# Kernel optimization log

Measured on AMD Instinct MI355X. Metric: run time of the kernel, lower is better.

Reference implementation:

```python
import jax, jax.numpy as jnp
import numpy as np

B, S, D, H, NK = 2, 512, 256, 8, 16
DK = D // H
NEG = -1e32


def _layer_norm(x, g, b, eps=1e-5):
    m = jnp.mean(x, axis=-1, keepdims=True)
    v = jnp.var(x, axis=-1, keepdims=True)
    return (x - m) / jnp.sqrt(v + eps) * g + b


def _attention(q, k, v, mask, gamma, maxout):
    # q,k,v: [b,h,s,dk]; mask: [1,1,s,s] bool; gamma: [h,1,1]
    d_k = q.shape[-1]
    scores = jnp.einsum('bhqd,bhkd->bhqk', q, k) / float(np.sqrt(d_k))
    s = scores.shape[-1]
    # gamma exp-decay branch (at=None in practice -> position_effect path)
    sm = jax.nn.softmax(jnp.where(mask, scores, NEG), axis=-1)
    distcum = jnp.cumsum(sm, axis=-1)
    disttotal = jnp.sum(sm, axis=-1, keepdims=True)
    idx = jnp.arange(s, dtype=scores.dtype)
    pos = jnp.abs(idx[None, :] - idx[:, None])[None, None]  # |x1 - x2|
    dist = jax.lax.stop_gradient(
        jnp.sqrt(jnp.clip((disttotal - distcum) * pos, 0.0, None)))
    g = -jnp.abs(gamma)[None]  # [1,h,1,1]
    total_effect = jnp.clip(jnp.exp(dist * g), 1e-5, 1e5)
    scores = scores * total_effect
    scores = jax.nn.softmax(jnp.where(mask, scores, NEG), axis=-1)
    scores = jnp.where(mask, scores, 0.0)
    if maxout:
        scale = jnp.minimum(1.0 / jnp.max(scores, axis=-1, keepdims=True), 5.0)
        scores = scores * scale
    out = jnp.einsum('bhqk,bhkd->bhqd', scores, v)
    return out, scores


def _mha(qx, kx, vx, mask, Wq, bq, Wk, bk, Wv, bv, Wo, bo, gammas, maxout):
    b, s, d = qx.shape
    def proj(x, W, bb):
        return (x @ W.T + bb).reshape(b, s, H, DK).transpose(0, 2, 1, 3)
    q = proj(qx, Wq, bq)
    k = proj(kx, Wk, bk)
    v = proj(vx, Wv, bv)
    out, scores = _attention(q, k, v, mask, gammas, maxout)
    concat = out.transpose(0, 2, 1, 3).reshape(b, s, d)
    return concat @ Wo.T + bo, scores


def _layer(qx, kx, vx, mask, Wq, bq, Wk, bk, Wv, bv, Wo, bo, gammas, ln_g, ln_b, maxout):
    out, scores = _mha(qx, kx, vx, mask, Wq, bq, Wk, bk, Wv, bv, Wo, bo, gammas, maxout)
    return _layer_norm(qx + out, ln_g, ln_b), scores  # dropout=identity in eval


def setup_inputs() -> dict:
    key = jax.random.key(0)
    ks = iter(jax.random.split(key, 40))
    def W(shp, sc=0.05):
        return jax.random.normal(next(ks), shp, jnp.float32) * sc
    return dict(
        q_emb=jax.random.normal(next(ks), (B, S, D), jnp.float32),
        s_emb=jax.random.normal(next(ks), (B, S, D), jnp.float32),
        s_emb_extr=jax.random.normal(next(ks), (B, S, D), jnp.float32),
        lens=jax.random.randint(next(ks), (B,), 1, S),
        at=jax.random.randint(next(ks), (B, S), 0, 300),
        Wq1=W((D, D)), bq1=jnp.zeros((D,)), Wv1=W((D, D)), bv1=jnp.zeros((D,)),
        Wo1=W((D, D)), bo1=jnp.zeros((D,)), gam1=W((H, 1, 1), 0.3),
        ln1_g=jnp.ones((D,)), ln1_b=jnp.zeros((D,)),
        Wq4=W((D, D)), bq4=jnp.zeros((D,)), Wk4=W((D, D)), bk4=jnp.zeros((D,)),
        Wv4=W((D, D)), bv4=jnp.zeros((D,)),
        Wo4=W((D, D)), bo4=jnp.zeros((D,)), gam4=W((H, 1, 1), 0.3),
        ln4_g=jnp.ones((D,)), ln4_b=jnp.zeros((D,)),
        know_params=jax.random.uniform(next(ks), (NK, D), jnp.float32, -1.0, 1.0),
    )


def reference(q_emb, s_emb, s_emb_extr, lens, at,
              Wq1, bq1, Wv1, bv1, Wo1, bo1, gam1, ln1_g, ln1_b,
              Wq4, bq4, Wk4, bk4, Wv4, bv4, Wo4, bo4, gam4, ln4_g, ln4_b,
              know_params):
    bs, s, d = q_emb.shape
    tri = jnp.tril(jnp.ones((s, s), bool), 0)[None, None]       # peek_cur=True
    tri_strict = jnp.tril(jnp.ones((s, s), bool), -1)[None, None]  # peek_cur=False
    # block1: kq_same -> k_linear is q_linear; maxout=False
    p, q_scores = _layer(q_emb, q_emb, s_emb, tri,
                         Wq1, bq1, Wq1, bq1, Wv1, bv1, Wo1, bo1, gam1,
                         ln1_g, ln1_b, maxout=False)
    # expand knowledge queries: [bs*NK, s, d]
    query = jnp.broadcast_to(know_params[None, :, None, :], (bs, NK, s, d)).reshape(bs * NK, s, d)
    hq = jnp.broadcast_to(q_emb[:, None], (bs, NK, s, d)).reshape(bs * NK, s, d)
    pe = jnp.broadcast_to(p[:, None], (bs, NK, s, d)).reshape(bs * NK, s, d)
    # block4: kq_same=False; maxout=True
    z, k_scores = _layer(query, hq, pe, tri_strict,
                         Wq4, bq4, Wk4, bk4, Wv4, bv4, Wo4, bo4, gam4,
                         ln4_g, ln4_b, maxout=True)
    z = z.reshape(bs, NK, s, d).transpose(0, 2, 1, 3).reshape(bs, s, NK * d)
    k_scores = k_scores.reshape(bs, NK, H, s, s).transpose(0, 2, 3, 1, 4)
    return z, q_scores, k_scores
```

## Files before the change

kernel.cpp:

```cpp
#include <hip/hip_runtime.h>


namespace {
constexpr int kB = 2, kS = 512, kD = 256, kH = 8, kDK = 32, kNK = 16;
constexpr float kScale = 0.17677669529663687f;
constexpr int kPS = 520;
constexpr int kSL = 528;
}

typedef unsigned short u16;
typedef u16 u16x4 __attribute__((ext_vector_type(4)));
typedef u16 u16x8 __attribute__((ext_vector_type(8)));
typedef short s16x8 __attribute__((ext_vector_type(8)));
typedef float f32x4 __attribute__((ext_vector_type(4)));

__device__ __forceinline__ float bf2f(u16 u) { return __uint_as_float(((unsigned)u) << 16); }
__device__ __forceinline__ u16 f2bf(float f) {
    unsigned u = __float_as_uint(f);
    return (u16)((u + 0x7fffu + ((u >> 16) & 1u)) >> 16);
}

__device__ __forceinline__ float wave_max64(float v) {
#pragma unroll
    for (int off = 32; off; off >>= 1) v = fmaxf(v, __shfl_xor(v, off));
    return v;
}
__device__ __forceinline__ float wave_sum64(float v) {
#pragma unroll
    for (int off = 32; off; off >>= 1) v += __shfl_xor(v, off);
    return v;
}

__global__ __launch_bounds__(256) void wt_kernel(const float* __restrict__ W0,
                                                 const float* __restrict__ W1,
                                                 const float* __restrict__ W2,
                                                 const float* __restrict__ W3,
                                                 const float* __restrict__ W4,
                                                 const float* __restrict__ W5,
                                                 const float* __restrict__ W6,
                                                 float* __restrict__ WT) {
    __shared__ float tile[32][33];
    const float* srcs[7] = {W0, W1, W2, W3, W4, W5, W6};
    const float* W = srcs[blockIdx.y];
    float* T = WT + (size_t)blockIdx.y * kD * kD;
    const int tx = blockIdx.x & 7, ty = blockIdx.x >> 3;
    const int t = threadIdx.x;
    {
        const int cl = t >> 3, kl = (t & 7) * 4;
        f32x4 v = *(const f32x4*)(W + (size_t)(ty * 32 + cl) * kD + tx * 32 + kl);
        tile[cl][kl] = v[0]; tile[cl][kl + 1] = v[1];
        tile[cl][kl + 2] = v[2]; tile[cl][kl + 3] = v[3];
    }
    __syncthreads();
    {
        const int kl = t >> 3, cl = (t & 7) * 4;
        f32x4 o = {tile[cl][kl], tile[cl + 1][kl], tile[cl + 2][kl], tile[cl + 3][kl]};
        *(f32x4*)(T + (size_t)(tx * 32 + kl) * kD + ty * 32 + cl) = o;
    }
}

__global__ __launch_bounds__(256) void gemm256_b4(const float* __restrict__ q_emb,
                                                  const float* __restrict__ s_emb,
                                                  const float* __restrict__ know,
                                                  const float* __restrict__ WTq1,
                                                  const float* __restrict__ bq1,
                                                  const float* __restrict__ WTv1,
                                                  const float* __restrict__ bv1,
                                                  const float* __restrict__ WTk4,
                                                  const float* __restrict__ bk4,
                                                  const float* __restrict__ WTq4,
                                                  const float* __restrict__ bq4,
                                                  float* __restrict__ Q1,
                                                  u16* __restrict__ Vtg1,
                                                  float* __restrict__ K4,
                                                  float* __restrict__ Q4) {
    const int mode = blockIdx.y;
    if (mode == 3 && blockIdx.x >= 4) return;
    __shared__ float xs[4][kD];
    const float* X = (mode == 1) ? s_emb : (mode == 3) ? know : q_emb;
    const float* WT = (mode == 0) ? WTq1 : (mode == 1) ? WTv1 : (mode == 2) ? WTk4 : WTq4;
    const float* bias = (mode == 0) ? bq1 : (mode == 1) ? bv1 : (mode == 2) ? bk4 : bq4;
    const int t = threadIdx.x;
    const int r0 = blockIdx.x * 4;

    {
        const int idx = t * 4;
        const int r = idx >> 8, c = idx & 255;
        *(f32x4*)&xs[r][c] = *(const f32x4*)(X + (size_t)(r0 + r) * kD + c);
    }
    __syncthreads();

    const int wv = t >> 6;
    const int c4 = (t & 63) * 4;
    float acc[4];
    {
        f32x4 bv = *(const f32x4*)(bias + c4);
#pragma unroll
        for (int j = 0; j < 4; ++j) acc[j] = bv[j];
    }
    for (int k0 = 0; k0 < kD; k0 += 4) {
        f32x4 w0 = *(const f32x4*)(WT + (size_t)(k0 + 0) * kD + c4);
        f32x4 w1 = *(const f32x4*)(WT + (size_t)(k0 + 1) * kD + c4);
        f32x4 w2 = *(const f32x4*)(WT + (size_t)(k0 + 2) * kD + c4);
        f32x4 w3 = *(const f32x4*)(WT + (size_t)(k0 + 3) * kD + c4);
        f32x4 xv = *(const f32x4*)&xs[wv][k0];
#pragma unroll
        for (int cc = 0; cc < 4; ++cc) {
            acc[cc] = fmaf(xv[0], w0[cc], acc[cc]);
            acc[cc] = fmaf(xv[1], w1[cc], acc[cc]);
            acc[cc] = fmaf(xv[2], w2[cc], acc[cc]);
            acc[cc] = fmaf(xv[3], w3[cc], acc[cc]);
        }
    }
    const int row = r0 + wv;
    if (mode == 3) {
        *(f32x4*)(Q4 + (size_t)row * kD + c4) = *(f32x4*)acc;
    } else if (mode == 1) {
        const int b = row >> 9, s = row & (kS - 1);
        const int h = c4 >> 5, dk = c4 & 31;
        u16* base = Vtg1 + (((size_t)(b * kH + h) * kDK + dk) * kS + s);
#pragma unroll
        for (int j = 0; j < 4; ++j) base[(size_t)j * kS] = f2bf(acc[j]);
    } else {
        float* Y = (mode == 0) ? Q1 : K4;
        const int h = c4 >> 5, dk = c4 & 31;
        *(f32x4*)(Y + (((size_t)(row >> 9) * kH + h) * kS + (row & (kS - 1))) * kDK + dk) =
            *(f32x4*)acc;
    }
}

__global__ __launch_bounds__(256) void epi1v4_kernel(const float* __restrict__ A1,
                                                     const float* __restrict__ qe,
                                                     const float* __restrict__ WTo1,
                                                     const float* __restrict__ bo1,
                                                     const float* __restrict__ lng,
                                                     const float* __restrict__ lnb,
                                                     const float* __restrict__ WTv4,
                                                     const float* __restrict__ bv4,
                                                     u16* __restrict__ Vtg) {
    __shared__ float xs[4][kD];
    __shared__ float ps[4][kD];
    const int t = threadIdx.x;
    const int r0 = blockIdx.x * 4;

    {
        const int chunk = t >> 3;
        const int r = chunk >> 3, h = chunk & 7;
        const int row = r0 + r;
        const float* src = A1 + (((size_t)(row >> 9) * kH + h) * kS + (row & (kS - 1))) * kDK + (t & 7) * 4;
        *(f32x4*)&xs[r][h * kDK + (t & 7) * 4] = *(const f32x4*)src;
    }
    __syncthreads();

    const int wv = t >> 6;
    const int c4 = (t & 63) * 4;
    const int row = r0 + wv;

    {
        float acc[4];
        f32x4 bv = *(const f32x4*)(bo1 + c4);
#pragma unroll
        for (int j = 0; j < 4; ++j) acc[j] = bv[j];
        for (int k0 = 0; k0 < kD; k0 += 4) {
            f32x4 w0 = *(const f32x4*)(WTo1 + (size_t)(k0 + 0) * kD + c4);
            f32x4 w1 = *(const f32x4*)(WTo1 + (size_t)(k0 + 1) * kD + c4);
            f32x4 w2 = *(const f32x4*)(WTo1 + (size_t)(k0 + 2) * kD + c4);
            f32x4 w3 = *(const f32x4*)(WTo1 + (size_t)(k0 + 3) * kD + c4);
            f32x4 xv = *(const f32x4*)&xs[wv][k0];
#pragma unroll
            for (int cc = 0; cc < 4; ++cc) {
                acc[cc] = fmaf(xv[0], w0[cc], acc[cc]);
                acc[cc] = fmaf(xv[1], w1[cc], acc[cc]);
                acc[cc] = fmaf(xv[2], w2[cc], acc[cc]);
                acc[cc] = fmaf(xv[3], w3[cc], acc[cc]);
            }
        }
        f32x4 e = *(const f32x4*)(qe + (size_t)row * kD + c4);
        f32x4 x;
#pragma unroll
        for (int j = 0; j < 4; ++j) x[j] = acc[j] + e[j];
        float s1 = x[0] + x[1] + x[2] + x[3];
        float s2 = x[0] * x[0] + x[1] * x[1] + x[2] * x[2] + x[3] * x[3];
#pragma unroll
        for (int off = 32; off; off >>= 1) {
            s1 += __shfl_xor(s1, off);
            s2 += __shfl_xor(s2, off);
        }
        const float mean = s1 * (1.f / kD);
        const float var = s2 * (1.f / kD) - mean * mean;
        const float rstd = rsqrtf(var + 1e-5f);
        f32x4 g = *(const f32x4*)(lng + c4);
        f32x4 bb = *(const f32x4*)(lnb + c4);
#pragma unroll
        for (int j = 0; j < 4; ++j) ps[wv][c4 + j] = (x[j] - mean) * rstd * g[j] + bb[j];
    }
    __syncthreads();

    {
        float acc[4];
        f32x4 bv = *(const f32x4*)(bv4 + c4);
#pragma unroll
        for (int j = 0; j < 4; ++j) acc[j] = bv[j];
        for (int k0 = 0; k0 < kD; k0 += 4) {
            f32x4 w0 = *(const f32x4*)(WTv4 + (size_t)(k0 + 0) * kD + c4);
            f32x4 w1 = *(const f32x4*)(WTv4 + (size_t)(k0 + 1) * kD + c4);
            f32x4 w2 = *(const f32x4*)(WTv4 + (size_t)(k0 + 2) * kD + c4);
            f32x4 w3 = *(const f32x4*)(WTv4 + (size_t)(k0 + 3) * kD + c4);
            f32x4 xv = *(const f32x4*)&ps[wv][k0];
#pragma unroll
            for (int cc = 0; cc < 4; ++cc) {
                acc[cc] = fmaf(xv[0], w0[cc], acc[cc]);
                acc[cc] = fmaf(xv[1], w1[cc], acc[cc]);
                acc[cc] = fmaf(xv[2], w2[cc], acc[cc]);
                acc[cc] = fmaf(xv[3], w3[cc], acc[cc]);
            }
        }
        const int b = row >> 9, s = row & (kS - 1);
        const int h = c4 >> 5, dk = c4 & 31;
        u16* base = Vtg + (((size_t)(b * kH + h) * kDK + dk) * kS + s);
#pragma unroll
        for (int j = 0; j < 4; ++j) base[(size_t)j * kS] = f2bf(acc[j]);
    }
}

template <int RPW, int MODE>
__global__ __launch_bounds__(256) void gemm256(const float* __restrict__ X,
                                               const float* __restrict__ WT,
                                               const float* __restrict__ bias,
                                               const float* __restrict__ extra,
                                               const float* __restrict__ lng,
                                               const float* __restrict__ lnb,
                                               float* __restrict__ Y) {
    constexpr int TM = RPW * 4;
    __shared__ float xs[TM][kD];
    const int t = threadIdx.x;
    const int r0 = blockIdx.x * TM;

    if (MODE == 0) {
#pragma unroll
        for (int it = 0; it < RPW; ++it) {
            const int idx = it * 1024 + t * 4;
            const int r = idx >> 8, c = idx & 255;
            *(f32x4*)&xs[r][c] = *(const f32x4*)(X + (size_t)(r0 + r) * kD + c);
        }
    } else {
#pragma unroll
        for (int it = 0; it < RPW; ++it) {
            const int chunk = it * 32 + (t >> 3);
            const int r = chunk >> 3, h = chunk & 7;
            const int row = r0 + r;
            const float* src = X + (((size_t)(row >> 9) * kH + h) * kS + (row & (kS - 1))) * kDK + (t & 7) * 4;
            *(f32x4*)&xs[r][h * kDK + (t & 7) * 4] = *(const f32x4*)src;
        }
    }
    __syncthreads();

    const int wv = t >> 6;
    const int c4 = (t & 63) * 4;
    float acc[RPW][4];
    {
        f32x4 bv = *(const f32x4*)(bias + c4);
#pragma unroll
        for (int r = 0; r < RPW; ++r)
#pragma unroll
            for (int j = 0; j < 4; ++j) acc[r][j] = bv[j];
    }
    for (int k0 = 0; k0 < kD; k0 += 4) {
        f32x4 w0 = *(const f32x4*)(WT + (size_t)(k0 + 0) * kD + c4);
        f32x4 w1 = *(const f32x4*)(WT + (size_t)(k0 + 1) * kD + c4);
        f32x4 w2 = *(const f32x4*)(WT + (size_t)(k0 + 2) * kD + c4);
        f32x4 w3 = *(const f32x4*)(WT + (size_t)(k0 + 3) * kD + c4);
#pragma unroll
        for (int r = 0; r < RPW; ++r) {
            f32x4 xv = *(const f32x4*)&xs[wv * RPW + r][k0];
#pragma unroll
            for (int cc = 0; cc < 4; ++cc) {
                acc[r][cc] = fmaf(xv[0], w0[cc], acc[r][cc]);
                acc[r][cc] = fmaf(xv[1], w1[cc], acc[r][cc]);
                acc[r][cc] = fmaf(xv[2], w2[cc], acc[r][cc]);
                acc[r][cc] = fmaf(xv[3], w3[cc], acc[r][cc]);
            }
        }
    }

#pragma unroll
    for (int r = 0; r < RPW; ++r) {
        const int row = r0 + wv * RPW + r;
        if (MODE == 0) {
            const int h = c4 >> 5, dk = c4 & 31;
            *(f32x4*)(Y + (((size_t)(row >> 9) * kH + h) * kS + (row & (kS - 1))) * kDK + dk) =
                *(f32x4*)acc[r];
        } else {
            f32x4 x;
            if (MODE == 1) {
                f32x4 e = *(const f32x4*)(extra + (size_t)row * kD + c4);
#pragma unroll
                for (int j = 0; j < 4; ++j) x[j] = acc[r][j] + e[j];
            } else {
                const int nk = (row >> 9) & (kNK - 1);
                f32x4 e = *(const f32x4*)(extra + (size_t)nk * kD + c4);
#pragma unroll
                for (int j = 0; j < 4; ++j) x[j] = acc[r][j] + e[j];
            }
            float s1 = x[0] + x[1] + x[2] + x[3];
            float s2 = x[0] * x[0] + x[1] * x[1] + x[2] * x[2] + x[3] * x[3];
#pragma unroll
            for (int off = 32; off; off >>= 1) {
                s1 += __shfl_xor(s1, off);
                s2 += __shfl_xor(s2, off);
            }
            const float mean = s1 * (1.f / kD);
            const float var = s2 * (1.f / kD) - mean * mean;
            const float rstd = rsqrtf(var + 1e-5f);
            f32x4 g = *(const f32x4*)(lng + c4);
            f32x4 bb = *(const f32x4*)(lnb + c4);
            f32x4 y;
#pragma unroll
            for (int j = 0; j < 4; ++j) y[j] = (x[j] - mean) * rstd * g[j] + bb[j];
            if (MODE == 1) {
                *(f32x4*)(Y + (size_t)row * kD + c4) = y;
            } else {
                const int bnk = row >> 9, s = row & (kS - 1);
                const int nk = bnk & (kNK - 1), b = bnk >> 4;
                *(f32x4*)(Y + (((size_t)(b * kS + s) * kNK + nk) * kD) + c4) = y;
            }
        }
    }
}

__global__ __launch_bounds__(256) void attn1_kernel(const float* __restrict__ Q1,
                                                    const u16* __restrict__ Vtg1,
                                                    const float* __restrict__ gam,
                                                    float* __restrict__ q_scores,
                                                    float* __restrict__ A1) {
    extern __shared__ char smem[];
    float* Sl = (float*)smem;
    u16* Pl = (u16*)smem;

    const int bh = blockIdx.x;
    const int q0 = blockIdx.y * 16;
    const int h = bh & (kH - 1);
    const int tid = threadIdx.x;
    const int lane = tid & 63;
    const int w = tid >> 6;
    const float* Kb = Q1 + (size_t)bh * kS * kDK;

    {
        const int qrow = q0 + (lane & 15);
        const int dof = (lane >> 4) * 8;
        f32x4 qa = *(const f32x4*)(Kb + (size_t)qrow * kDK + dof);
        f32x4 qb = *(const f32x4*)(Kb + (size_t)qrow * kDK + dof + 4);
        s16x8 aq_h, aq_l;
#pragma unroll
        for (int j = 0; j < 4; ++j) {
            float f = qa[j];
            u16 hi = f2bf(f);
            aq_h[j] = (short)hi;
            aq_l[j] = (short)f2bf(f - bf2f(hi));
            f = qb[j];
            hi = f2bf(f);
            aq_h[4 + j] = (short)hi;
            aq_l[4 + j] = (short)f2bf(f - bf2f(hi));
        }
        for (int kt = w * 8; kt < w * 8 + 8; ++kt) {
            const int krow = kt * 16 + (lane & 15);
            f32x4 ka = *(const f32x4*)(Kb + (size_t)krow * kDK + dof);
            f32x4 kb2 = *(const f32x4*)(Kb + (size_t)krow * kDK + dof + 4);
            s16x8 bk_h, bk_l;
#pragma unroll
            for (int j = 0; j < 4; ++j) {
                float f = ka[j];
                u16 hi = f2bf(f);
                bk_h[j] = (short)hi;
                bk_l[j] = (short)f2bf(f - bf2f(hi));
                f = kb2[j];
                hi = f2bf(f);
                bk_h[4 + j] = (short)hi;
                bk_l[4 + j] = (short)f2bf(f - bf2f(hi));
            }
            f32x4 acc = {0.f, 0.f, 0.f, 0.f};
            acc = __builtin_amdgcn_mfma_f32_16x16x32_bf16(aq_h, bk_h, acc, 0, 0, 0);
            acc = __builtin_amdgcn_mfma_f32_16x16x32_bf16(aq_l, bk_h, acc, 0, 0, 0);
            acc = __builtin_amdgcn_mfma_f32_16x16x32_bf16(aq_h, bk_l, acc, 0, 0, 0);
            const int colk = kt * 16 + (lane & 15);
            const int seg = colk >> 5, ii = colk & 31;
#pragma unroll
            for (int j = 0; j < 4; ++j) {
                const int row = (lane >> 4) * 4 + j;
                Sl[row * kSL + seg * 33 + ii] = acc[j] * kScale;
            }
        }
    }
    __syncthreads();

    const float gh = -fabsf(gam[h]);
    const int r = tid >> 4, seg16 = tid & 15;
    const int q = q0 + r, L = q + 1, ks = seg16 * 32;
    float sv[32];
    {
        const float* srow = Sl + r * kSL + seg16 * 33;
#pragma unroll
        for (int i = 0; i < 32; ++i) sv[i] = srow[i];
    }
    __syncthreads();
    {
        const int nv = min(max(L - ks, 0), 32);
        float m = -3e38f;
#pragma unroll
        for (int i = 0; i < 32; ++i)
            if (i < nv) m = fmaxf(m, sv[i]);
#pragma unroll
        for (int off = 1; off < 16; off <<= 1) m = fmaxf(m, __shfl_xor(m, off));
        float segsum = 0.f;
#pragma unroll
        for (int i = 0; i < 32; ++i)
            if (i < nv) segsum += __expf(sv[i] - m);
        float tot = segsum;
#pragma unroll
        for (int off = 1; off < 16; off <<= 1) tot += __shfl_xor(tot, off);
        float inc = segsum;
#pragma unroll
        for (int off = 1; off < 16; off <<= 1) {
            const float tmp = __shfl_up(inc, off);
            if ((tid & 15) >= off) inc += tmp;
        }
        float run = inc - segsum;
        const float inv_tot = 1.f / tot;
        float m2 = -3e38f;
#pragma unroll
        for (int i = 0; i < 32; ++i) {
            if (i < nv) {
                const float E = __expf(sv[i] - m);
                run += E;
                const float rem = 1.f - run * inv_tot;
                const float pos = (float)(q - (ks + i));
                const float val = fmaxf(rem * pos, 0.f);
                const float te = fmaxf(__expf(gh * sqrtf(val)), 1e-5f);
                const float s2 = sv[i] * te;
                sv[i] = s2;
                m2 = fmaxf(m2, s2);
            }
        }
#pragma unroll
        for (int off = 1; off < 16; off <<= 1) m2 = fmaxf(m2, __shfl_xor(m2, off));
        float sum2 = 0.f;
#pragma unroll
        for (int i = 0; i < 32; ++i) {
            const float p = (i < nv) ? __expf(sv[i] - m2) : 0.f;
            sv[i] = p;
            sum2 += p;
        }
#pragma unroll
        for (int off = 1; off < 16; off <<= 1) sum2 += __shfl_xor(sum2, off);
        const float inv2 = 1.f / sum2;
        float* qrow = q_scores + ((size_t)bh * kS + q) * kS + ks;
        u16* prow = Pl + r * kPS + ks;
#pragma unroll
        for (int i = 0; i < 32; i += 4) {
            f32x4 o;
            u16x4 pb;
#pragma unroll
            for (int j = 0; j < 4; ++j) {
                const float p = sv[i + j] * inv2;
                o[j] = p;
                pb[j] = f2bf(p);
            }
            *(f32x4*)(qrow + i) = o;
            *(u16x4*)(prow + i) = pb;
        }
    }
    __syncthreads();

    if (w < 2) {
        const int dt = w;
        const u16* Arow = Pl + (size_t)(lane & 15) * kPS + (lane >> 4) * 8;
        const u16* Brow = Vtg1 + ((size_t)bh * kDK + dt * 16 + (lane & 15)) * kS + (lane >> 4) * 8;
        f32x4 acc = {0.f, 0.f, 0.f, 0.f};
#pragma unroll
        for (int kc = 0; kc < kS; kc += 32) {
            s16x8 a = *(const s16x8*)(Arow + kc);
            s16x8 b = *(const s16x8*)(Brow + kc);
            acc = __builtin_amdgcn_mfma_f32_16x16x32_bf16(a, b, acc, 0, 0, 0);
        }
        const int d = dt * 16 + (lane & 15);
#pragma unroll
        for (int j = 0; j < 4; ++j) {
            const int row = (lane >> 4) * 4 + j;
            A1[((size_t)bh * kS + (q0 + row)) * kDK + d] = acc[j];
        }
    }
}

__global__ __launch_bounds__(64) void attn4_prep(const float* __restrict__ Q4,
                                                 const float* __restrict__ K4,
                                                 float* __restrict__ rawP,
                                                 float* __restrict__ CpreP) {
    const int panel = blockIdx.x;
    const int h = panel & (kH - 1);
    const int bnk = panel >> 3;
    const int nk = bnk & (kNK - 1);
    const int b = bnk >> 4;
    const int lane = threadIdx.x;
    const float* Kp = K4 + (size_t)(b * kH + h) * kS * kDK;
    float qv[kDK];
    const float* Qr = Q4 + (size_t)nk * kD + h * kDK;
#pragma unroll
    for (int d = 0; d < kDK; ++d) qv[d] = Qr[d];

    const int k0 = lane * 8;
    float raw[8];
    float m = -3e38f;
#pragma unroll
    for (int j = 0; j < 8; ++j) {
        const float* kr = Kp + (size_t)(k0 + j) * kDK;
        float s = 0.f;
#pragma unroll
        for (int d4 = 0; d4 < 8; ++d4) {
            f32x4 kv = *(const f32x4*)(kr + d4 * 4);
            s = fmaf(qv[d4 * 4 + 0], kv[0], s);
            s = fmaf(qv[d4 * 4 + 1], kv[1], s);
            s = fmaf(qv[d4 * 4 + 2], kv[2], s);
            s = fmaf(qv[d4 * 4 + 3], kv[3], s);
        }
        raw[j] = s * kScale;
        m = fmaxf(m, raw[j]);
    }
    m = wave_max64(m);
    float E[8];
    float s = 0.f;
#pragma unroll
    for (int j = 0; j < 8; ++j) { E[j] = __expf(raw[j] - m); s += E[j]; }
    float inc = s;
#pragma unroll
    for (int off = 1; off < 64; off <<= 1) {
        float t = __shfl_up(inc, off);
        if (lane >= off) inc += t;
    }
    float run = inc - s;
    float cp[8];
#pragma unroll
    for (int j = 0; j < 8; ++j) { run += E[j]; cp[j] = run; }

    float* rrow = rawP + (size_t)panel * kS + k0;
    float* crow = CpreP + (size_t)panel * kS + k0;
    *(f32x4*)(rrow) = *(f32x4*)(raw);
    *(f32x4*)(rrow + 4) = *(f32x4*)(raw + 4);
    *(f32x4*)(crow) = *(f32x4*)(cp);
    *(f32x4*)(crow + 4) = *(f32x4*)(cp + 4);
}

__global__ __launch_bounds__(256) void attn4_main(const float* __restrict__ rawP,
                                                  const float* __restrict__ CpreP,
                                                  const u16* __restrict__ Vtg,
                                                  const float* __restrict__ gam,
                                                  float* __restrict__ k_scores,
                                                  float* __restrict__ A4) {
    extern __shared__ char smem[];
    u16* Pl = (u16*)smem;
    float* raws_l = (float*)(smem + 32 * kPS * 2);
    float* cps_l = raws_l + kS;

    const int panel = blockIdx.x;
    const int q0 = blockIdx.y * 32;
    const int h = panel & (kH - 1);
    const int bnk = panel >> 3;
    const int nk = bnk & (kNK - 1);
    const int b = bnk >> 4;
    const int tid = threadIdx.x;
    const int lane = tid & 63;
    const int w = tid >> 6;

    for (int i = tid; i < kS; i += 256) {
        raws_l[i] = rawP[(size_t)panel * kS + i];
        cps_l[i] = CpreP[(size_t)panel * kS + i];
    }
    __syncthreads();

    const float gh = -fabsf(gam[h]);
    const int rbase = w * 8;
    const int k0 = lane * 8;
    float rw[8], cp[8];
    *(f32x4*)(rw) = *(const f32x4*)(raws_l + k0);
    *(f32x4*)(rw + 4) = *(const f32x4*)(raws_l + k0 + 4);
    *(f32x4*)(cp) = *(const f32x4*)(cps_l + k0);
    *(f32x4*)(cp + 4) = *(const f32x4*)(cps_l + k0 + 4);

    for (int r = 0; r < 8; ++r) {
        const int row = rbase + r;
        const int Lr = q0 + row;
        float* krow = k_scores + ((size_t)((b * kH + h) * kS + Lr) * kNK + nk) * kS;
        u16* prow = Pl + (size_t)row * kPS + k0;
        if (Lr == 0) {
            f32x4 z = {0.f, 0.f, 0.f, 0.f};
            *(f32x4*)(krow + k0) = z;
            *(f32x4*)(krow + k0 + 4) = z;
            u16x8 zb = {0, 0, 0, 0, 0, 0, 0, 0};
            *(u16x8*)(prow) = zb;
            continue;
        }
        const float invCL = 1.f / cps_l[Lr - 1];
        const float fL = (float)(Lr - k0);
        float s2v[8];
        float mloc = -3e38f;
#pragma unroll
        for (int j = 0; j < 8; ++j) {
            const float rem = 1.f - cp[j] * invCL;
            const float val = fmaxf(rem * (fL - (float)j), 0.f);
            const float te = fmaxf(__expf(gh * sqrtf(val)), 1e-5f);
            const float s2 = rw[j] * te;
            s2v[j] = s2;
            if (k0 + j < Lr) mloc = fmaxf(mloc, s2);
        }
        const float m2 = wave_max64(mloc);
        float p[8];
        float psum = 0.f;
#pragma unroll
        for (int j = 0; j < 8; ++j) {
            p[j] = (k0 + j < Lr) ? __expf(s2v[j] - m2) : 0.f;
            psum += p[j];
        }
        const float sum2 = wave_sum64(psum);
        const float scl = fminf(sum2, 5.f) / sum2;
        u16x8 pb;
#pragma unroll
        for (int j = 0; j < 8; ++j) {
            p[j] *= scl;
            pb[j] = f2bf(p[j]);
        }
        *(f32x4*)(krow + k0) = *(f32x4*)(p);
        *(f32x4*)(krow + k0 + 4) = *(f32x4*)(p + 4);
        *(u16x8*)(prow) = pb;
    }
    __syncthreads();

    const int rowblk = (w & 1) * 16;
    const int dblk = (w >> 1) * 16;
    const u16* Arow = Pl + (size_t)(rowblk + (lane & 15)) * kPS + (lane >> 4) * 8;
    const u16* Brow = Vtg + ((size_t)(b * kH + h) * kDK + dblk + (lane & 15)) * kS + (lane >> 4) * 8;
    f32x4 acc = {0.f, 0.f, 0.f, 0.f};
#pragma unroll
    for (int kc = 0; kc < kS; kc += 32) {
        s16x8 a = *(const s16x8*)(Arow + kc);
        s16x8 bfr = *(const s16x8*)(Brow + kc);
        acc = __builtin_amdgcn_mfma_f32_16x16x32_bf16(a, bfr, acc, 0, 0, 0);
    }
    const int d = dblk + (lane & 15);
#pragma unroll
    for (int j = 0; j < 4; ++j) {
        const int row = rowblk + (lane >> 4) * 4 + j;
        A4[((size_t)panel * kS + (q0 + row)) * kDK + d] = acc[j];
    }
}

extern "C" void kernel_launch(void* const* d_in, const int* in_sizes, int n_in,
                              void* d_out, int out_size, void* d_ws, size_t ws_size,
                              hipStream_t stream) {
    (void)in_sizes; (void)n_in; (void)out_size; (void)ws_size;

    const float* q_emb = (const float*)d_in[0];
    const float* s_emb = (const float*)d_in[1];
    const float* Wq1 = (const float*)d_in[5];  const float* bq1 = (const float*)d_in[6];
    const float* Wv1 = (const float*)d_in[7];  const float* bv1 = (const float*)d_in[8];
    const float* Wo1 = (const float*)d_in[9];  const float* bo1 = (const float*)d_in[10];
    const float* gam1 = (const float*)d_in[11];
    const float* ln1g = (const float*)d_in[12]; const float* ln1b = (const float*)d_in[13];
    const float* Wq4 = (const float*)d_in[14]; const float* bq4 = (const float*)d_in[15];
    const float* Wk4 = (const float*)d_in[16]; const float* bk4 = (const float*)d_in[17];
    const float* Wv4 = (const float*)d_in[18]; const float* bv4 = (const float*)d_in[19];
    const float* Wo4 = (const float*)d_in[20]; const float* bo4 = (const float*)d_in[21];
    const float* gam4 = (const float*)d_in[22];
    const float* ln4g = (const float*)d_in[23]; const float* ln4b = (const float*)d_in[24];
    const float* know = (const float*)d_in[25];

    float* ws = (float*)d_ws;
    const size_t NBHSD = (size_t)kB * kH * kS * kDK;
    float* Q1 = ws;
    float* RAW = Q1 + NBHSD;
    float* A1 = RAW + NBHSD;
    float* K4 = A1 + NBHSD;
    float* Q4 = K4 + NBHSD;
    float* A4 = Q4 + (size_t)kNK * kD;
    float* WT = A4 + (size_t)kB * kNK * kH * kS * kDK;
    u16* Vtg = (u16*)(WT + 7 * (size_t)kD * kD);
    u16* Vtg1 = Vtg + (size_t)kB * kH * kDK * kS;

    float* rawP = RAW;
    float* CpreP = RAW + (size_t)kB * kNK * kH * kS;

    float* WTq1 = WT + 0 * (size_t)kD * kD;
    float* WTv1 = WT + 1 * (size_t)kD * kD;
    float* WTo1 = WT + 2 * (size_t)kD * kD;
    float* WTk4 = WT + 3 * (size_t)kD * kD;
    float* WTv4 = WT + 4 * (size_t)kD * kD;
    float* WTo4 = WT + 5 * (size_t)kD * kD;
    float* WTq4 = WT + 6 * (size_t)kD * kD;

    float* zout = (float*)d_out;
    float* q_scores = zout + (size_t)kB * kS * kNK * kD;
    float* k_scores = q_scores + (size_t)kB * kH * kS * kS;

    {
        dim3 g(64, 7);
        wt_kernel<<<g, 256, 0, stream>>>(Wq1, Wv1, Wo1, Wk4, Wv4, Wo4, Wq4, WT);
    }
    {
        dim3 g(kB * kS / 4, 4);
        gemm256_b4<<<g, 256, 0, stream>>>(q_emb, s_emb, know,
                                          WTq1, bq1, WTv1, bv1, WTk4, bk4, WTq4, bq4,
                                          Q1, Vtg1, K4, Q4);
    }
    attn4_prep<<<kB * kNK * kH, 64, 0, stream>>>(Q4, K4, rawP, CpreP);
    {
        dim3 g1(kB * kH, kS / 16);
        const int lds1 = 16 * kSL * 4;
        attn1_kernel<<<g1, 256, lds1, stream>>>(Q1, Vtg1, gam1, q_scores, A1);
    }
    epi1v4_kernel<<<kB * kS / 4, 256, 0, stream>>>(A1, q_emb, WTo1, bo1, ln1g, ln1b,
                                                   WTv4, bv4, Vtg);
    {
        dim3 g5(kB * kNK * kH, kS / 32);
        const int lds_bytes = 32 * kPS * 2 + 2 * kS * 4;
        attn4_main<<<g5, 256, lds_bytes, stream>>>(rawP, CpreP, Vtg, gam4, k_scores, A4);
    }
    gemm256<4, 2><<<kB * kNK * kS / 16, 256, 0, stream>>>(A4, WTo4, bo4, know, ln4g, ln4b, zout);
}
```

Baseline: 218.7 us.

## Merge attn4_prep into attn1 launch and use nontemporal stores for score outputs

The separate attn4_prep kernel is folded into the attn1 kernel as extra blocks in a flattened 1-D grid. Each of the four waves in those extra blocks handles one panel, which removes one launch and lets the prep work overlap with attention-1 blocks. Large write-only outputs (q_scores, k_scores and the final z) now use nontemporal stores so they do not pollute the cache. The prep blocks reserve the full attn1 LDS allocation they never use, which may limit occupancy. Nontemporal stores can also behave differently depending on how the hardware handles them.

```diff
diff --git a/kernel.cpp b/kernel.cpp
--- a/kernel.cpp
+++ b/kernel.cpp
@@ -18,6 +18,9 @@
 __device__ __forceinline__ u16 f2bf(float f) {
     unsigned u = __float_as_uint(f);
     return (u16)((u + 0x7fffu + ((u >> 16) & 1u)) >> 16);
+}
+__device__ __forceinline__ void nt_store4(float* p, f32x4 v) {
+    __builtin_nontemporal_store(v, (f32x4*)p);
 }
 
 __device__ __forceinline__ float wave_max64(float v) {
@@ -322,27 +325,88 @@
             } else {
                 const int bnk = row >> 9, s = row & (kS - 1);
                 const int nk = bnk & (kNK - 1), b = bnk >> 4;
-                *(f32x4*)(Y + (((size_t)(b * kS + s) * kNK + nk) * kD) + c4) = y;
-            }
-        }
-    }
-}
-
-__global__ __launch_bounds__(256) void attn1_kernel(const float* __restrict__ Q1,
-                                                    const u16* __restrict__ Vtg1,
-                                                    const float* __restrict__ gam,
-                                                    float* __restrict__ q_scores,
-                                                    float* __restrict__ A1) {
+                nt_store4(Y + (((size_t)(b * kS + s) * kNK + nk) * kD) + c4, y);
+            }
+        }
+    }
+}
+
+__global__ __launch_bounds__(256) void attn1_prep_kernel(const float* __restrict__ Q1,
+                                                         const u16* __restrict__ Vtg1,
+                                                         const float* __restrict__ gam,
+                                                         const float* __restrict__ Q4,
+                                                         const float* __restrict__ K4,
+                                                         float* __restrict__ rawP,
+                                                         float* __restrict__ CpreP,
+                                                         float* __restrict__ q_scores,
+                                                         float* __restrict__ A1) {
     extern __shared__ char smem[];
-    float* Sl = (float*)smem;
-    u16* Pl = (u16*)smem;
-
-    const int bh = blockIdx.x;
-    const int q0 = blockIdx.y * 16;
-    const int h = bh & (kH - 1);
+    const int bx = blockIdx.x;
     const int tid = threadIdx.x;
     const int lane = tid & 63;
     const int w = tid >> 6;
+
+    if (bx >= kB * kH * (kS / 16)) {
+        const int panel = (bx - kB * kH * (kS / 16)) * 4 + w;
+        const int h = panel & (kH - 1);
+        const int bnk = panel >> 3;
+        const int nk = bnk & (kNK - 1);
+        const int b = bnk >> 4;
+        const float* Kp = K4 + (size_t)(b * kH + h) * kS * kDK;
+        float qv[kDK];
+        const float* Qr = Q4 + (size_t)nk * kD + h * kDK;
+#pragma unroll
+        for (int d = 0; d < kDK; ++d) qv[d] = Qr[d];
+
+        const int k0 = lane * 8;
+        float raw[8];
+        float m = -3e38f;
+#pragma unroll
+        for (int j = 0; j < 8; ++j) {
+            const float* kr = Kp + (size_t)(k0 + j) * kDK;
+            float s = 0.f;
+#pragma unroll
+            for (int d4 = 0; d4 < 8; ++d4) {
+                f32x4 kv = *(const f32x4*)(kr + d4 * 4);
+                s = fmaf(qv[d4 * 4 + 0], kv[0], s);
+                s = fmaf(qv[d4 * 4 + 1], kv[1], s);
+                s = fmaf(qv[d4 * 4 + 2], kv[2], s);
+                s = fmaf(qv[d4 * 4 + 3], kv[3], s);
+            }
+            raw[j] = s * kScale;
+            m = fmaxf(m, raw[j]);
+        }
+        m = wave_max64(m);
+        float E[8];
+        float s = 0.f;
+#pragma unroll
+        for (int j = 0; j < 8; ++j) { E[j] = __expf(raw[j] - m); s += E[j]; }
+        float inc = s;
+#pragma unroll
+        for (int off = 1; off < 64; off <<= 1) {
+            float t2 = __shfl_up(inc, off);
+            if (lane >= off) inc += t2;
+        }
+        float run = inc - s;
+        float cp[8];
+#pragma unroll
+        for (int j = 0; j < 8; ++j) { run += E[j]; cp[j] = run; }
+
+        float* rrow = rawP + (size_t)panel * kS + k0;
+        float* crow = CpreP + (size_t)panel * kS + k0;
+        *(f32x4*)(rrow) = *(f32x4*)(raw);
+        *(f32x4*)(rrow + 4) = *(f32x4*)(raw + 4);
+        *(f32x4*)(crow) = *(f32x4*)(cp);
+        *(f32x4*)(crow + 4) = *(f32x4*)(cp + 4);
+        return;
+    }
+
+    float* Sl = (float*)smem;
+    u16* Pl = (u16*)smem;
+
+    const int bh = bx >> 5;
+    const int q0 = (bx & 31) * 16;
+    const int h = bh & (kH - 1);
     const float* Kb = Q1 + (size_t)bh * kS * kDK;
 
     {
@@ -465,7 +529,7 @@
                 o[j] = p;
                 pb[j] = f2bf(p);
             }
-            *(f32x4*)(qrow + i) = o;
+            nt_store4(qrow + i, o);
             *(u16x4*)(prow + i) = pb;
         }
     }
@@ -489,64 +553,6 @@
             A1[((size_t)bh * kS + (q0 + row)) * kDK + d] = acc[j];
         }
     }
-}
-
-__global__ __launch_bounds__(64) void attn4_prep(const float* __restrict__ Q4,
-                                                 const float* __restrict__ K4,
-                                                 float* __restrict__ rawP,
-                                                 float* __restrict__ CpreP) {
-    const int panel = blockIdx.x;
-    const int h = panel & (kH - 1);
-    const int bnk = panel >> 3;
-    const int nk = bnk & (kNK - 1);
-    const int b = bnk >> 4;
-    const int lane = threadIdx.x;
-    const float* Kp = K4 + (size_t)(b * kH + h) * kS * kDK;
-    float qv[kDK];
-    const float* Qr = Q4 + (size_t)nk * kD + h * kDK;
-#pragma unroll
-    for (int d = 0; d < kDK; ++d) qv[d] = Qr[d];
-
-    const int k0 = lane * 8;
-    float raw[8];
-    float m = -3e38f;
-#pragma unroll
-    for (int j = 0; j < 8; ++j) {
-        const float* kr = Kp + (size_t)(k0 + j) * kDK;
-        float s = 0.f;
-#pragma unroll
-        for (int d4 = 0; d4 < 8; ++d4) {
-            f32x4 kv = *(const f32x4*)(kr + d4 * 4);
-            s = fmaf(qv[d4 * 4 + 0], kv[0], s);
-            s = fmaf(qv[d4 * 4 + 1], kv[1], s);
-            s = fmaf(qv[d4 * 4 + 2], kv[2], s);
-            s = fmaf(qv[d4 * 4 + 3], kv[3], s);
-        }
-        raw[j] = s * kScale;
-        m = fmaxf(m, raw[j]);
-    }
-    m = wave_max64(m);
-    float E[8];
-    float s = 0.f;
-#pragma unroll
-    for (int j = 0; j < 8; ++j) { E[j] = __expf(raw[j] - m); s += E[j]; }
-    float inc = s;
-#pragma unroll
-    for (int off = 1; off < 64; off <<= 1) {
-        float t = __shfl_up(inc, off);
-        if (lane >= off) inc += t;
-    }
-    float run = inc - s;
-    float cp[8];
-#pragma unroll
-    for (int j = 0; j < 8; ++j) { run += E[j]; cp[j] = run; }
-
-    float* rrow = rawP + (size_t)panel * kS + k0;
-    float* crow = CpreP + (size_t)panel * kS + k0;
-    *(f32x4*)(rrow) = *(f32x4*)(raw);
-    *(f32x4*)(rrow + 4) = *(f32x4*)(raw + 4);
-    *(f32x4*)(crow) = *(f32x4*)(cp);
-    *(f32x4*)(crow + 4) = *(f32x4*)(cp + 4);
 }
 
 __global__ __launch_bounds__(256) void attn4_main(const float* __restrict__ rawP,
@@ -592,8 +598,8 @@
         u16* prow = Pl + (size_t)row * kPS + k0;
         if (Lr == 0) {
             f32x4 z = {0.f, 0.f, 0.f, 0.f};
-            *(f32x4*)(krow + k0) = z;
-            *(f32x4*)(krow + k0 + 4) = z;
+            nt_store4(krow + k0, z);
+            nt_store4(krow + k0 + 4, z);
             u16x8 zb = {0, 0, 0, 0, 0, 0, 0, 0};
             *(u16x8*)(prow) = zb;
             continue;
@@ -627,8 +633,8 @@
             p[j] *= scl;
             pb[j] = f2bf(p[j]);
         }
-        *(f32x4*)(krow + k0) = *(f32x4*)(p);
-        *(f32x4*)(krow + k0 + 4) = *(f32x4*)(p + 4);
+        nt_store4(krow + k0, *(f32x4*)(p));
+        nt_store4(krow + k0 + 4, *(f32x4*)(p + 4));
         *(u16x8*)(prow) = pb;
     }
     __syncthreads();
@@ -709,11 +715,12 @@
                                           WTq1, bq1, WTv1, bv1, WTk4, bk4, WTq4, bq4,
                                           Q1, Vtg1, K4, Q4);
     }
-    attn4_prep<<<kB * kNK * kH, 64, 0, stream>>>(Q4, K4, rawP, CpreP);
-    {
-        dim3 g1(kB * kH, kS / 16);
+    {
+        const int nb1 = kB * kH * (kS / 16);
+        const int nbp = kB * kNK * kH / 4;
         const int lds1 = 16 * kSL * 4;
-        attn1_kernel<<<g1, 256, lds1, stream>>>(Q1, Vtg1, gam1, q_scores, A1);
+        attn1_prep_kernel<<<nb1 + nbp, 256, lds1, stream>>>(Q1, Vtg1, gam1, Q4, K4,
+                                                            rawP, CpreP, q_scores, A1);
     }
     epi1v4_kernel<<<kB * kS / 4, 256, 0, stream>>>(A1, q_emb, WTo1, bo1, ln1g, ln1b,
                                                    WTv4, bv4, Vtg);
```

New measurement: 236.0 us. 1.08x slower.
